# Kernel tuning notes

Hardware: AMD Instinct MI355X
Metric: run time of the kernel (lower is better)

## Reference

```python
import jax, jax.numpy as jnp
import numpy as np
import math

IN_FEATURES = 4096
OUT_FEATURES = 4096
RANK = 16
B, S = 4, 2048


def setup_inputs() -> dict:
    key = jax.random.key(0)
    k_x, k_w, k_b, k_a = jax.random.split(key, 4)
    x = jax.random.normal(k_x, (B, S, IN_FEATURES), dtype=jnp.float32)
    # base linear params (torch nn.Linear default init scale)
    bound_w = 1.0 / math.sqrt(IN_FEATURES)
    W = jax.random.uniform(k_w, (OUT_FEATURES, IN_FEATURES), minval=-bound_w, maxval=bound_w, dtype=jnp.float32)
    bias = jax.random.uniform(k_b, (OUT_FEATURES,), minval=-bound_w, maxval=bound_w, dtype=jnp.float32)
    # lora_A: kaiming_uniform_(a=sqrt(5)) over shape (out, rank) -> fan_in = rank
    bound_a = 1.0 / math.sqrt(RANK)
    lora_A = jax.random.uniform(k_a, (OUT_FEATURES, RANK), minval=-bound_a, maxval=bound_a, dtype=jnp.float32)
    # lora_B initialized to zeros in the module; use small random values so the
    # delta path is numerically exercised in the baseline.
    lora_B = jax.random.normal(jax.random.fold_in(key, 7), (RANK, IN_FEATURES), dtype=jnp.float32) * 0.01
    return {"x": x, "W": W, "bias": bias, "lora_A": lora_A, "lora_B": lora_B}


def reference(x, W, bias, lora_A, lora_B):
    # Faithful to the torch module: materialize the full [out, in] LoRA delta
    # (lora_A @ lora_B), then apply base linear + delta linear.
    lora_update = lora_A @ lora_B                      # [out, in]
    base = jnp.einsum('bsi,oi->bso', x, W) + bias      # base_layer(x)
    delta = jnp.einsum('bsi,oi->bso', x, lora_update)  # F.linear(x, lora_update)
    return base + delta
```

## Files before the change

### kernel.cpp

```cpp
#include <hip/hip_runtime.h>
#include <hip/hip_bf16.h>
#include <stdint.h>


typedef unsigned short u16;
typedef __attribute__((ext_vector_type(8))) u16 u16x8;
typedef __attribute__((ext_vector_type(4))) u16 u16x4;
typedef __attribute__((ext_vector_type(8))) __bf16 bf16x8;
typedef __attribute__((ext_vector_type(4))) float f32x4;

#define IN_F 4096
#define OUT_F 4096
#define MTOT 8192
#define RANK 16
#define NTILE 384

__device__ __forceinline__ u16 f2bf(float f) {
  unsigned u = __float_as_uint(f);
  unsigned r = u + 0x7FFFu + ((u >> 16) & 1u);
  return (u16)(r >> 16);
}
__device__ __forceinline__ float bf2f(u16 h) {
  return __uint_as_float(((unsigned)h) << 16);
}

__global__ __launch_bounds__(256) void split_x_kernel(
    const float* __restrict__ x, u16* __restrict__ hi, u16* __restrict__ lo,
    int n4) {
  int idx = blockIdx.x * blockDim.x + threadIdx.x;
  const int stride = gridDim.x * blockDim.x;
  for (; idx < n4; idx += stride) {
    float4 v = ((const float4*)x)[idx];
    u16x4 h, l;
    h.x = f2bf(v.x); l.x = f2bf(v.x - bf2f(h.x));
    h.y = f2bf(v.y); l.y = f2bf(v.y - bf2f(h.y));
    h.z = f2bf(v.z); l.z = f2bf(v.z - bf2f(h.z));
    h.w = f2bf(v.w); l.w = f2bf(v.w - bf2f(h.w));
    ((u16x4*)hi)[idx] = h;
    ((u16x4*)lo)[idx] = l;
  }
}

__global__ __launch_bounds__(256) void build_w_kernel(
    const float* __restrict__ W, const float* __restrict__ lA,
    const float* __restrict__ lB, u16* __restrict__ whi,
    u16* __restrict__ wlo) {
  const int o = blockIdx.x * 2 + (threadIdx.x >> 7);
  const int tl = threadIdx.x & 127;
  float a[RANK];
#pragma unroll
  for (int r = 0; r < RANK; ++r) a[r] = lA[o * RANK + r];
  const float4* W4 = (const float4*)(W + (size_t)o * IN_F);
  u16x4* h4 = (u16x4*)(whi + (size_t)o * IN_F);
  u16x4* l4 = (u16x4*)(wlo + (size_t)o * IN_F);
  for (int i4 = tl; i4 < IN_F / 4; i4 += 128) {
    float4 acc = W4[i4];
#pragma unroll
    for (int r = 0; r < RANK; ++r) {
      float4 b = ((const float4*)(lB + (size_t)r * IN_F))[i4];
      acc.x += a[r] * b.x; acc.y += a[r] * b.y;
      acc.z += a[r] * b.z; acc.w += a[r] * b.w;
    }
    u16x4 h, l;
    h.x = f2bf(acc.x); l.x = f2bf(acc.x - bf2f(h.x));
    h.y = f2bf(acc.y); l.y = f2bf(acc.y - bf2f(h.y));
    h.z = f2bf(acc.z); l.z = f2bf(acc.z - bf2f(h.z));
    h.w = f2bf(acc.w); l.w = f2bf(acc.w - bf2f(h.w));
    h4[i4] = h; l4[i4] = l;
  }
}

#define GLD_LDS16(g, l)                                                  \
  __builtin_amdgcn_global_load_lds(                                      \
      (const __attribute__((address_space(1))) void*)(g),                \
      (__attribute__((address_space(3))) void*)(l), 16, 0, 0)

__global__ __launch_bounds__(512, 2) void gemm_pipe_kernel(
    const u16* __restrict__ Xhi, const u16* __restrict__ Xlo,
    const u16* __restrict__ Whi, const u16* __restrict__ Wlo,
    const float* __restrict__ bias, float* __restrict__ out) {
  __shared__ __align__(16) u16 LDS[4 * 16384];

  const int t = threadIdx.x;
  const int lane = t & 63;
  const int wv = t >> 6;
  const int wm = wv >> 2;
  const int wn = wv & 3;
  const int fr = lane & 15;
  const int fq = lane >> 4;

  const int wg = ((blockIdx.x & 7) << 6) | (blockIdx.x >> 3);
  const int m0 = (wg >> 4) * 256;
  const int n0 = (wg & 15) * 256;

  const int srow = t >> 2;
  const int scol = ((t & 3) ^ ((t >> 3) & 3)) * 8;
  const size_t a_off0 = (size_t)(m0 + srow) * IN_F + scol;
  const size_t a_off1 = (size_t)(m0 + 128 + srow) * IN_F + scol;
  const size_t b_off0 = (size_t)(n0 + srow) * IN_F + scol;
  const size_t b_off1 = (size_t)(n0 + 128 + srow) * IN_F + scol;
  const int sdst0 = t * 8;
  const int sdst1 = 4096 + t * 8;

  const int swz = (fq ^ ((fr >> 1) & 3)) * 8;
  const int a_rd = (wm * 128 + fr) * 32 + swz;
  const int b_rd = (wn * 64 + fr) * 32 + swz;

  f32x4 acc[8][4];
#pragma unroll
  for (int i = 0; i < 8; ++i)
#pragma unroll
    for (int j = 0; j < 4; ++j) {
      acc[i][j][0] = 0.f; acc[i][j][1] = 0.f;
      acc[i][j][2] = 0.f; acc[i][j][3] = 0.f;
    }

  auto stageA = [&](int g, int buf) {
    const int sg = g >> 7;
    const u16* ap = (sg == 1) ? Xlo : Xhi;
    const int k0 = (g & 127) << 5;
    u16* dst = (u16*)&LDS[buf * 16384];
    GLD_LDS16(ap + a_off0 + k0, dst + sdst0);
    GLD_LDS16(ap + a_off1 + k0, dst + sdst1);
  };
  auto stageB = [&](int g, int buf) {
    const int sg = g >> 7;
    const u16* bp = (sg == 2) ? Wlo : Whi;
    const int k0 = (g & 127) << 5;
    u16* dst = (u16*)&LDS[buf * 16384 + 8192];
    GLD_LDS16(bp + b_off0 + k0, dst + sdst0);
    GLD_LDS16(bp + b_off1 + k0, dst + sdst1);
  };

  stageA(0, 0); stageB(0, 0);
  stageA(1, 1); stageB(1, 1);
  stageA(2, 2); stageB(2, 2);

#pragma unroll 1
  for (int tt = 0; tt < NTILE; ++tt) {
    const int buf = tt & 3;
    const u16* Ab = &LDS[buf * 16384];
    const u16* Bb = Ab + 8192;
    int g = tt + 3;
    if (g >= NTILE) g = NTILE - 1;
    const int pbuf = (tt + 3) & 3;

    asm volatile("s_waitcnt vmcnt(8)" ::: "memory");
    __builtin_amdgcn_s_barrier();
    __builtin_amdgcn_sched_barrier(0);

    u16x8 af[4], bf[4];
#pragma unroll
    for (int mi = 0; mi < 4; ++mi)
      af[mi] = *(const u16x8*)&Ab[a_rd + mi * 512];
#pragma unroll
    for (int ni = 0; ni < 4; ++ni)
      bf[ni] = *(const u16x8*)&Bb[b_rd + ni * 512];
    stageA(g, pbuf);
    asm volatile("s_waitcnt lgkmcnt(0)" ::: "memory");
    __builtin_amdgcn_sched_barrier(0);
    __builtin_amdgcn_s_setprio(1);
#pragma unroll
    for (int mi = 0; mi < 4; ++mi)
#pragma unroll
      for (int ni = 0; ni < 4; ++ni)
        acc[mi][ni] = __builtin_amdgcn_mfma_f32_16x16x32_bf16(
            __builtin_bit_cast(bf16x8, af[mi]),
            __builtin_bit_cast(bf16x8, bf[ni]), acc[mi][ni], 0, 0, 0);
    __builtin_amdgcn_s_setprio(0);
    __builtin_amdgcn_s_barrier();

#pragma unroll
    for (int mi = 0; mi < 4; ++mi)
      af[mi] = *(const u16x8*)&Ab[a_rd + 2048 + mi * 512];
    stageB(g, pbuf);
    asm volatile("s_waitcnt lgkmcnt(0)" ::: "memory");
    __builtin_amdgcn_sched_barrier(0);
    __builtin_amdgcn_s_setprio(1);
#pragma unroll
    for (int mi = 0; mi < 4; ++mi)
#pragma unroll
      for (int ni = 0; ni < 4; ++ni)
        acc[4 + mi][ni] = __builtin_amdgcn_mfma_f32_16x16x32_bf16(
            __builtin_bit_cast(bf16x8, af[mi]),
            __builtin_bit_cast(bf16x8, bf[ni]), acc[4 + mi][ni], 0, 0, 0);
    __builtin_amdgcn_s_setprio(0);
  }

#pragma unroll
  for (int mig = 0; mig < 8; ++mig) {
    const int row = m0 + wm * 128 + mig * 16 + fq * 4;
#pragma unroll
    for (int ni = 0; ni < 4; ++ni) {
      const int col = n0 + wn * 64 + ni * 16 + fr;
      const float bb = bias[col];
#pragma unroll
      for (int r = 0; r < 4; ++r)
        out[(size_t)(row + r) * OUT_F + col] = acc[mig][ni][r] + bb;
    }
  }
}

__global__ __launch_bounds__(256) void gemm_f32_fallback(
    const float* __restrict__ X, const float* __restrict__ W,
    const float* __restrict__ lA, const float* __restrict__ lB,
    const float* __restrict__ bias, float* __restrict__ out) {
  __shared__ __align__(16) float Xs[64 * 32];
  __shared__ __align__(16) float Ws[64 * 32];
  const int t = threadIdx.x;
  const int bm = blockIdx.x & 127;
  const int bn = blockIdx.x >> 7;
  const int m0 = bm * 64, n0 = bn * 64;
  const int tx = t & 15, ty = t >> 4;
  float acc[4][4] = {};
  for (int k0 = 0; k0 < IN_F; k0 += 32) {
    __syncthreads();
#pragma unroll
    for (int q = 0; q < 2; ++q) {
      const int e4 = t * 2 + q;
      const int row = e4 >> 3;
      const int col = (e4 & 7) * 4;
      float4 xv = *(const float4*)(X + (size_t)(m0 + row) * IN_F + k0 + col);
      *(float4*)(Xs + row * 32 + col) = xv;
      float4 wv = *(const float4*)(W + (size_t)(n0 + row) * IN_F + k0 + col);
#pragma unroll
      for (int r = 0; r < RANK; ++r) {
        const float a = lA[(n0 + row) * RANK + r];
        const float4 b = *(const float4*)(lB + (size_t)r * IN_F + k0 + col);
        wv.x += a * b.x; wv.y += a * b.y; wv.z += a * b.z; wv.w += a * b.w;
      }
      *(float4*)(Ws + row * 32 + col) = wv;
    }
    __syncthreads();
#pragma unroll
    for (int kk = 0; kk < 32; ++kk) {
      float xr[4], wcol[4];
#pragma unroll
      for (int i = 0; i < 4; ++i) xr[i] = Xs[(ty * 4 + i) * 32 + kk];
#pragma unroll
      for (int j = 0; j < 4; ++j) wcol[j] = Ws[(tx * 4 + j) * 32 + kk];
#pragma unroll
      for (int i = 0; i < 4; ++i)
#pragma unroll
        for (int j = 0; j < 4; ++j) acc[i][j] += xr[i] * wcol[j];
    }
  }
#pragma unroll
  for (int i = 0; i < 4; ++i) {
    const int row = m0 + ty * 4 + i;
#pragma unroll
    for (int j = 0; j < 4; ++j) {
      const int col = n0 + tx * 4 + j;
      out[(size_t)row * OUT_F + col] = acc[i][j] + bias[col];
    }
  }
}

extern "C" void kernel_launch(void* const* d_in, const int* in_sizes, int n_in,
                              void* d_out, int out_size, void* d_ws,
                              size_t ws_size, hipStream_t stream) {
  const float* x    = (const float*)d_in[0];
  const float* W    = (const float*)d_in[1];
  const float* bias = (const float*)d_in[2];
  const float* lA   = (const float*)d_in[3];
  const float* lB   = (const float*)d_in[4];
  float* out = (float*)d_out;

  const size_t MK = (size_t)MTOT * IN_F;
  const size_t NK = (size_t)OUT_F * IN_F;
  const size_t need = (MK * 2 + NK * 2) * sizeof(u16);

  if (ws_size >= need) {
    u16* Xhi = (u16*)d_ws;
    u16* Xlo = Xhi + MK;
    u16* Whi = Xlo + MK;
    u16* Wlo = Whi + NK;
    split_x_kernel<<<4096, 256, 0, stream>>>(x, Xhi, Xlo, (int)(MK / 4));
    build_w_kernel<<<OUT_F / 2, 256, 0, stream>>>(W, lA, lB, Whi, Wlo);
    gemm_pipe_kernel<<<512, 512, 0, stream>>>(Xhi, Xlo, Whi, Wlo, bias, out);
  } else {
    gemm_f32_fallback<<<128 * 64, 256, 0, stream>>>(x, W, lA, lB, bias, out);
  }
}
```

Baseline: 980.1 us.

## Switch GEMM to K=64 double-buffered tiles and merge prep kernels

The GEMM main loop now stages 64-wide K slices (192 iterations instead of 384) into two LDS buffers with a new 8-way XOR swizzle. Each iteration is split into four MFMA phases so global-to-LDS loads can overlap with compute. The split-x and build-W kernels are merged into one launch to cut launch overhead. Going from four buffers to two and waiting on vmcnt(0) gives a shallower prefetch, which may expose more memory latency.

```diff
diff --git a/kernel.cpp b/kernel.cpp
--- a/kernel.cpp
+++ b/kernel.cpp
@@ -13,7 +13,7 @@
 #define OUT_F 4096
 #define MTOT 8192
 #define RANK 16
-#define NTILE 384
+#define NT64 192
 
 __device__ __forceinline__ u16 f2bf(float f) {
   unsigned u = __float_as_uint(f);
@@ -24,49 +24,48 @@
   return __uint_as_float(((unsigned)h) << 16);
 }
 
-__global__ __launch_bounds__(256) void split_x_kernel(
-    const float* __restrict__ x, u16* __restrict__ hi, u16* __restrict__ lo,
-    int n4) {
-  int idx = blockIdx.x * blockDim.x + threadIdx.x;
-  const int stride = gridDim.x * blockDim.x;
-  for (; idx < n4; idx += stride) {
-    float4 v = ((const float4*)x)[idx];
-    u16x4 h, l;
-    h.x = f2bf(v.x); l.x = f2bf(v.x - bf2f(h.x));
-    h.y = f2bf(v.y); l.y = f2bf(v.y - bf2f(h.y));
-    h.z = f2bf(v.z); l.z = f2bf(v.z - bf2f(h.z));
-    h.w = f2bf(v.w); l.w = f2bf(v.w - bf2f(h.w));
-    ((u16x4*)hi)[idx] = h;
-    ((u16x4*)lo)[idx] = l;
-  }
-}
-
-__global__ __launch_bounds__(256) void build_w_kernel(
-    const float* __restrict__ W, const float* __restrict__ lA,
-    const float* __restrict__ lB, u16* __restrict__ whi,
+__global__ __launch_bounds__(256) void prep_kernel(
+    const float* __restrict__ x, const float* __restrict__ W,
+    const float* __restrict__ lA, const float* __restrict__ lB,
+    u16* __restrict__ xhi, u16* __restrict__ xlo, u16* __restrict__ whi,
     u16* __restrict__ wlo) {
-  const int o = blockIdx.x * 2 + (threadIdx.x >> 7);
-  const int tl = threadIdx.x & 127;
-  float a[RANK];
-#pragma unroll
-  for (int r = 0; r < RANK; ++r) a[r] = lA[o * RANK + r];
-  const float4* W4 = (const float4*)(W + (size_t)o * IN_F);
-  u16x4* h4 = (u16x4*)(whi + (size_t)o * IN_F);
-  u16x4* l4 = (u16x4*)(wlo + (size_t)o * IN_F);
-  for (int i4 = tl; i4 < IN_F / 4; i4 += 128) {
-    float4 acc = W4[i4];
-#pragma unroll
-    for (int r = 0; r < RANK; ++r) {
-      float4 b = ((const float4*)(lB + (size_t)r * IN_F))[i4];
-      acc.x += a[r] * b.x; acc.y += a[r] * b.y;
-      acc.z += a[r] * b.z; acc.w += a[r] * b.w;
-    }
-    u16x4 h, l;
-    h.x = f2bf(acc.x); l.x = f2bf(acc.x - bf2f(h.x));
-    h.y = f2bf(acc.y); l.y = f2bf(acc.y - bf2f(h.y));
-    h.z = f2bf(acc.z); l.z = f2bf(acc.z - bf2f(h.z));
-    h.w = f2bf(acc.w); l.w = f2bf(acc.w - bf2f(h.w));
-    h4[i4] = h; l4[i4] = l;
+  if (blockIdx.x < 2048) {
+    const int n4 = (MTOT * IN_F) / 4;
+    int idx = blockIdx.x * 256 + threadIdx.x;
+    for (; idx < n4; idx += 2048 * 256) {
+      float4 v = ((const float4*)x)[idx];
+      u16x4 h, l;
+      h.x = f2bf(v.x); l.x = f2bf(v.x - bf2f(h.x));
+      h.y = f2bf(v.y); l.y = f2bf(v.y - bf2f(h.y));
+      h.z = f2bf(v.z); l.z = f2bf(v.z - bf2f(h.z));
+      h.w = f2bf(v.w); l.w = f2bf(v.w - bf2f(h.w));
+      ((u16x4*)xhi)[idx] = h;
+      ((u16x4*)xlo)[idx] = l;
+    }
+  } else {
+    const int o = (blockIdx.x - 2048) * 2 + (threadIdx.x >> 7);
+    const int tl = threadIdx.x & 127;
+    float a[RANK];
+#pragma unroll
+    for (int r = 0; r < RANK; ++r) a[r] = lA[o * RANK + r];
+    const float4* W4 = (const float4*)(W + (size_t)o * IN_F);
+    u16x4* h4 = (u16x4*)(whi + (size_t)o * IN_F);
+    u16x4* l4 = (u16x4*)(wlo + (size_t)o * IN_F);
+    for (int i4 = tl; i4 < IN_F / 4; i4 += 128) {
+      float4 acc = W4[i4];
+#pragma unroll
+      for (int r = 0; r < RANK; ++r) {
+        float4 b = ((const float4*)(lB + (size_t)r * IN_F))[i4];
+        acc.x += a[r] * b.x; acc.y += a[r] * b.y;
+        acc.z += a[r] * b.z; acc.w += a[r] * b.w;
+      }
+      u16x4 h, l;
+      h.x = f2bf(acc.x); l.x = f2bf(acc.x - bf2f(h.x));
+      h.y = f2bf(acc.y); l.y = f2bf(acc.y - bf2f(h.y));
+      h.z = f2bf(acc.z); l.z = f2bf(acc.z - bf2f(h.z));
+      h.w = f2bf(acc.w); l.w = f2bf(acc.w - bf2f(h.w));
+      h4[i4] = h; l4[i4] = l;
+    }
   }
 }
 
@@ -79,7 +78,7 @@
     const u16* __restrict__ Xhi, const u16* __restrict__ Xlo,
     const u16* __restrict__ Whi, const u16* __restrict__ Wlo,
     const float* __restrict__ bias, float* __restrict__ out) {
-  __shared__ __align__(16) u16 LDS[4 * 16384];
+  __shared__ __align__(16) u16 LDS[65536];
 
   const int t = threadIdx.x;
   const int lane = t & 63;
@@ -93,18 +92,12 @@
   const int m0 = (wg >> 4) * 256;
   const int n0 = (wg & 15) * 256;
 
-  const int srow = t >> 2;
-  const int scol = ((t & 3) ^ ((t >> 3) & 3)) * 8;
-  const size_t a_off0 = (size_t)(m0 + srow) * IN_F + scol;
-  const size_t a_off1 = (size_t)(m0 + 128 + srow) * IN_F + scol;
-  const size_t b_off0 = (size_t)(n0 + srow) * IN_F + scol;
-  const size_t b_off1 = (size_t)(n0 + 128 + srow) * IN_F + scol;
-  const int sdst0 = t * 8;
-  const int sdst1 = 4096 + t * 8;
-
-  const int swz = (fq ^ ((fr >> 1) & 3)) * 8;
-  const int a_rd = (wm * 128 + fr) * 32 + swz;
-  const int b_rd = (wn * 64 + fr) * 32 + swz;
+  const int scol = ((t & 7) ^ ((t >> 3) & 7)) * 8;
+  const size_t aoff = (size_t)(m0 + (t >> 3)) * IN_F + scol;
+  const size_t boff = (size_t)(n0 + (t >> 3)) * IN_F + scol;
+
+  const int lk0 = fr * 64 + (((0 * 4 + fq) ^ (fr & 7)) * 8);
+  const int lk1 = fr * 64 + (((1 * 4 + fq) ^ (fr & 7)) * 8);
 
   f32x4 acc[8][4];
 #pragma unroll
@@ -115,90 +108,141 @@
       acc[i][j][2] = 0.f; acc[i][j][3] = 0.f;
     }
 
-  auto stageA = [&](int g, int buf) {
-    const int sg = g >> 7;
+  auto stageA = [&](int g, int sbuf) {
+    const int sg = g >> 6;
     const u16* ap = (sg == 1) ? Xlo : Xhi;
-    const int k0 = (g & 127) << 5;
-    u16* dst = (u16*)&LDS[buf * 16384];
-    GLD_LDS16(ap + a_off0 + k0, dst + sdst0);
-    GLD_LDS16(ap + a_off1 + k0, dst + sdst1);
+    const int k0 = (g & 63) << 6;
+    u16* dA = (u16*)&LDS[sbuf * 32768];
+    const u16* s = ap + aoff + k0;
+    GLD_LDS16(s, dA + t * 8);
+    GLD_LDS16(s + (size_t)64 * IN_F, dA + (512 + t) * 8);
+    GLD_LDS16(s + (size_t)128 * IN_F, dA + (1024 + t) * 8);
+    GLD_LDS16(s + (size_t)192 * IN_F, dA + (1536 + t) * 8);
   };
-  auto stageB = [&](int g, int buf) {
-    const int sg = g >> 7;
+  auto stageB0 = [&](int g, int sbuf) {
+    const int sg = g >> 6;
     const u16* bp = (sg == 2) ? Wlo : Whi;
-    const int k0 = (g & 127) << 5;
-    u16* dst = (u16*)&LDS[buf * 16384 + 8192];
-    GLD_LDS16(bp + b_off0 + k0, dst + sdst0);
-    GLD_LDS16(bp + b_off1 + k0, dst + sdst1);
+    const int k0 = (g & 63) << 6;
+    u16* dB = (u16*)&LDS[sbuf * 32768 + 16384];
+    const u16* s = bp + boff + k0;
+    GLD_LDS16(s, dB + t * 8);
+    GLD_LDS16(s + (size_t)64 * IN_F, dB + (512 + t) * 8);
   };
-
-  stageA(0, 0); stageB(0, 0);
-  stageA(1, 1); stageB(1, 1);
-  stageA(2, 2); stageB(2, 2);
+  auto stageB1 = [&](int g, int sbuf) {
+    const int sg = g >> 6;
+    const u16* bp = (sg == 2) ? Wlo : Whi;
+    const int k0 = (g & 63) << 6;
+    u16* dB = (u16*)&LDS[sbuf * 32768 + 16384];
+    const u16* s = bp + boff + k0;
+    GLD_LDS16(s + (size_t)128 * IN_F, dB + (1024 + t) * 8);
+    GLD_LDS16(s + (size_t)192 * IN_F, dB + (1536 + t) * 8);
+  };
+
+#define MFMA_Q(AIDX, BARR, BIDX, ACC)                                   \
+  ACC = __builtin_amdgcn_mfma_f32_16x16x32_bf16(                        \
+      __builtin_bit_cast(bf16x8, af[AIDX]),                             \
+      __builtin_bit_cast(bf16x8, BARR[BIDX]), ACC, 0, 0, 0)
+
+  stageA(0, 0); stageB0(0, 0); stageB1(0, 0);
 
 #pragma unroll 1
-  for (int tt = 0; tt < NTILE; ++tt) {
-    const int buf = tt & 3;
-    const u16* Ab = &LDS[buf * 16384];
-    const u16* Bb = Ab + 8192;
-    int g = tt + 3;
-    if (g >= NTILE) g = NTILE - 1;
-    const int pbuf = (tt + 3) & 3;
-
-    asm volatile("s_waitcnt vmcnt(8)" ::: "memory");
+  for (int tt = 0; tt < NT64; ++tt) {
+    const int buf = tt & 1;
+    const u16* Ab = &LDS[buf * 32768];
+    const u16* Bb = Ab + 16384;
+    int g = tt + 1;
+    if (g >= NT64) g = NT64 - 1;
+    const int sbuf = buf ^ 1;
+
+    asm volatile("s_waitcnt vmcnt(0)" ::: "memory");
     __builtin_amdgcn_s_barrier();
     __builtin_amdgcn_sched_barrier(0);
 
-    u16x8 af[4], bf[4];
-#pragma unroll
-    for (int mi = 0; mi < 4; ++mi)
-      af[mi] = *(const u16x8*)&Ab[a_rd + mi * 512];
-#pragma unroll
-    for (int ni = 0; ni < 4; ++ni)
-      bf[ni] = *(const u16x8*)&Bb[b_rd + ni * 512];
-    stageA(g, pbuf);
+    u16x8 af[8], bf0[4], bf1[4];
+
+#pragma unroll
+    for (int mi = 0; mi < 4; ++mi) {
+      af[mi * 2 + 0] = *(const u16x8*)&Ab[wm * 8192 + mi * 1024 + lk0];
+      af[mi * 2 + 1] = *(const u16x8*)&Ab[wm * 8192 + mi * 1024 + lk1];
+    }
+#pragma unroll
+    for (int ci = 0; ci < 2; ++ci) {
+      bf0[ci * 2 + 0] = *(const u16x8*)&Bb[wn * 4096 + ci * 1024 + lk0];
+      bf0[ci * 2 + 1] = *(const u16x8*)&Bb[wn * 4096 + ci * 1024 + lk1];
+    }
+    stageA(g, sbuf);
     asm volatile("s_waitcnt lgkmcnt(0)" ::: "memory");
     __builtin_amdgcn_sched_barrier(0);
     __builtin_amdgcn_s_setprio(1);
 #pragma unroll
     for (int mi = 0; mi < 4; ++mi)
 #pragma unroll
-      for (int ni = 0; ni < 4; ++ni)
-        acc[mi][ni] = __builtin_amdgcn_mfma_f32_16x16x32_bf16(
-            __builtin_bit_cast(bf16x8, af[mi]),
-            __builtin_bit_cast(bf16x8, bf[ni]), acc[mi][ni], 0, 0, 0);
+      for (int ci = 0; ci < 2; ++ci) {
+        MFMA_Q(mi * 2 + 0, bf0, ci * 2 + 0, acc[mi][ci]);
+        MFMA_Q(mi * 2 + 1, bf0, ci * 2 + 1, acc[mi][ci]);
+      }
     __builtin_amdgcn_s_setprio(0);
-    __builtin_amdgcn_s_barrier();
-
-#pragma unroll
-    for (int mi = 0; mi < 4; ++mi)
-      af[mi] = *(const u16x8*)&Ab[a_rd + 2048 + mi * 512];
-    stageB(g, pbuf);
+
+#pragma unroll
+    for (int ci = 0; ci < 2; ++ci) {
+      bf1[ci * 2 + 0] = *(const u16x8*)&Bb[wn * 4096 + 2048 + ci * 1024 + lk0];
+      bf1[ci * 2 + 1] = *(const u16x8*)&Bb[wn * 4096 + 2048 + ci * 1024 + lk1];
+    }
+    stageB0(g, sbuf);
     asm volatile("s_waitcnt lgkmcnt(0)" ::: "memory");
     __builtin_amdgcn_sched_barrier(0);
     __builtin_amdgcn_s_setprio(1);
 #pragma unroll
     for (int mi = 0; mi < 4; ++mi)
 #pragma unroll
-      for (int ni = 0; ni < 4; ++ni)
-        acc[4 + mi][ni] = __builtin_amdgcn_mfma_f32_16x16x32_bf16(
-            __builtin_bit_cast(bf16x8, af[mi]),
-            __builtin_bit_cast(bf16x8, bf[ni]), acc[4 + mi][ni], 0, 0, 0);
+      for (int ci = 0; ci < 2; ++ci) {
+        MFMA_Q(mi * 2 + 0, bf1, ci * 2 + 0, acc[mi][2 + ci]);
+        MFMA_Q(mi * 2 + 1, bf1, ci * 2 + 1, acc[mi][2 + ci]);
+      }
     __builtin_amdgcn_s_setprio(0);
-  }
-
-#pragma unroll
-  for (int mig = 0; mig < 8; ++mig) {
-    const int row = m0 + wm * 128 + mig * 16 + fq * 4;
-#pragma unroll
-    for (int ni = 0; ni < 4; ++ni) {
-      const int col = n0 + wn * 64 + ni * 16 + fr;
+
+#pragma unroll
+    for (int mi = 0; mi < 4; ++mi) {
+      af[mi * 2 + 0] = *(const u16x8*)&Ab[wm * 8192 + 4096 + mi * 1024 + lk0];
+      af[mi * 2 + 1] = *(const u16x8*)&Ab[wm * 8192 + 4096 + mi * 1024 + lk1];
+    }
+    stageB1(g, sbuf);
+    asm volatile("s_waitcnt lgkmcnt(0)" ::: "memory");
+    __builtin_amdgcn_sched_barrier(0);
+    __builtin_amdgcn_s_setprio(1);
+#pragma unroll
+    for (int mi = 0; mi < 4; ++mi)
+#pragma unroll
+      for (int ci = 0; ci < 2; ++ci) {
+        MFMA_Q(mi * 2 + 0, bf1, ci * 2 + 0, acc[4 + mi][2 + ci]);
+        MFMA_Q(mi * 2 + 1, bf1, ci * 2 + 1, acc[4 + mi][2 + ci]);
+      }
+    __builtin_amdgcn_s_setprio(0);
+
+    __builtin_amdgcn_s_setprio(1);
+#pragma unroll
+    for (int mi = 0; mi < 4; ++mi)
+#pragma unroll
+      for (int ci = 0; ci < 2; ++ci) {
+        MFMA_Q(mi * 2 + 0, bf0, ci * 2 + 0, acc[4 + mi][ci]);
+        MFMA_Q(mi * 2 + 1, bf0, ci * 2 + 1, acc[4 + mi][ci]);
+      }
+    __builtin_amdgcn_s_setprio(0);
+  }
+
+#pragma unroll
+  for (int a = 0; a < 8; ++a) {
+    const int row = m0 + wm * 128 + (a >> 2) * 64 + (a & 3) * 16 + fq * 4;
+#pragma unroll
+    for (int b = 0; b < 4; ++b) {
+      const int col = n0 + wn * 64 + (b >> 1) * 32 + (b & 1) * 16 + fr;
       const float bb = bias[col];
 #pragma unroll
       for (int r = 0; r < 4; ++r)
-        out[(size_t)(row + r) * OUT_F + col] = acc[mig][ni][r] + bb;
-    }
-  }
+        out[(size_t)(row + r) * OUT_F + col] = acc[a][b][r] + bb;
+    }
+  }
+#undef MFMA_Q
 }
 
 __global__ __launch_bounds__(256) void gemm_f32_fallback(
@@ -275,8 +319,7 @@
     u16* Xlo = Xhi + MK;
     u16* Whi = Xlo + MK;
     u16* Wlo = Whi + NK;
-    split_x_kernel<<<4096, 256, 0, stream>>>(x, Xhi, Xlo, (int)(MK / 4));
-    build_w_kernel<<<OUT_F / 2, 256, 0, stream>>>(W, lA, lB, Whi, Wlo);
+    prep_kernel<<<4096, 256, 0, stream>>>(x, W, lA, lB, Xhi, Xlo, Whi, Wlo);
     gemm_pipe_kernel<<<512, 512, 0, stream>>>(Xhi, Xlo, Whi, Wlo, bias, out);
   } else {
     gemm_f32_fallback<<<128 * 64, 256, 0, stream>>>(x, W, lA, lB, bias, out);
```

New measurement: 910.6 us. 1.08x faster.
